# Kernel tuning notes

Hardware: AMD Instinct MI355X
Metric: run time of the kernel (lower is better)

The kernel has to match this reference:

```python
import math
import jax, jax.numpy as jnp
import numpy as np

B, S, E, H = 4, 2048, 1024, 16
HD = E // H  # 64


def setup_inputs() -> dict:
    key = jax.random.key(0)
    ks = jax.random.split(key, 7)
    scale = 1.0 / math.sqrt(E)
    return {
        "x": jax.random.normal(ks[0], (B, S, E), dtype=jnp.float32),
        "Wq": jax.random.normal(ks[1], (H, HD, E), dtype=jnp.float32) * scale,
        "bq": jax.random.normal(ks[2], (H, HD), dtype=jnp.float32) * 0.01,
        "Wk": jax.random.normal(ks[3], (H, HD, E), dtype=jnp.float32) * scale,
        "bk": jax.random.normal(ks[4], (H, HD), dtype=jnp.float32) * 0.01,
        "Wv": jax.random.normal(ks[5], (H, HD, E), dtype=jnp.float32) * scale,
        "bv": jax.random.normal(ks[6], (H, HD), dtype=jnp.float32) * 0.01,
    }


def reference(x, Wq, bq, Wk, bk, Wv, bv):
    b, s, e = x.shape
    h, hd, _ = Wq.shape
    inv_scale = 1.0 / math.sqrt(hd)
    # per-head linear projections (torch Linear: x @ W^T + b), batched over heads
    q = jnp.einsum("bse,hde->bshd", x, Wq) + bq  # [B,S,H,HD]
    k = jnp.einsum("bse,hde->bshd", x, Wk) + bk
    v = jnp.einsum("bse,hde->bshd", x, Wv) + bv
    # causal mask: -inf above diagonal (added before scaling, as in source;
    # -inf * inv_scale is still -inf so math is identical)
    mask = jnp.triu(jnp.full((s, s), -jnp.inf, dtype=x.dtype), k=1)
    scores = (jnp.einsum("bqhd,bkhd->bhqk", q, k) + mask) * inv_scale  # [B,H,S,S]
    attn = jax.nn.softmax(scores, axis=-1)
    out = jnp.einsum("bhqk,bkhd->bqhd", attn, v)  # [B,S,H,HD]
    # concat over heads in head order == reshape with head-major last dims
    return out.reshape(b, s, h * hd)
```

## Files before the change

### kernel.cpp

```cpp
#include <hip/hip_runtime.h>


typedef __bf16 bf16x8 __attribute__((ext_vector_type(8)));
typedef __bf16 bf16x4 __attribute__((ext_vector_type(4)));
typedef float f32x4 __attribute__((ext_vector_type(4)));
typedef unsigned short us8 __attribute__((ext_vector_type(8)));
typedef unsigned short us4 __attribute__((ext_vector_type(4)));

#define Bb 4
#define Ss 2048
#define Ee 1024
#define Hh 16
#define HD 64

#if __has_builtin(__builtin_amdgcn_exp2f)
#define EXP2(x) __builtin_amdgcn_exp2f(x)
#else
#define EXP2(x) exp2f(x)
#endif

__device__ __forceinline__ unsigned short f2bf(float f) {
  union { float f; unsigned u; } v; v.f = f;
  unsigned u = v.u;
  u += 0x7fffu + ((u >> 16) & 1u);
  return (unsigned short)(u >> 16);
}

__device__ __forceinline__ void gl_lds16(const void* g, void* l) {
  __builtin_amdgcn_global_load_lds((const __attribute__((address_space(1))) void*)g,
                                   (__attribute__((address_space(3))) void*)l, 16, 0, 0);
}

#define DSR(d, a, o) asm volatile("ds_read_b128 %0, %1 offset:" #o : "=v"(d) : "v"(a))
#define DSW(a, d, o) asm volatile("ds_write_b64 %0, %1 offset:" #o :: "v"(a), "v"(d) : "memory")
#define LGKM0 asm volatile("s_waitcnt lgkmcnt(0)" ::: "memory"); __builtin_amdgcn_sched_barrier(0)
#define LGKM8 asm volatile("s_waitcnt lgkmcnt(8)" ::: "memory"); __builtin_amdgcn_sched_barrier(0)

__global__ __launch_bounds__(256) void cvt_all(const float* __restrict__ x,
                                               const float* __restrict__ wq,
                                               const float* __restrict__ wk,
                                               const float* __restrict__ wv,
                                               unsigned short* __restrict__ xb,
                                               unsigned short* __restrict__ wb) {
  int i = blockIdx.x * 256 + threadIdx.x;
  const float* src; unsigned short* dst; int idx;
  if (i < 2097152)      { src = x;  dst = xb;                idx = i; }
  else if (i < 2359296) { src = wq; dst = wb;                idx = i - 2097152; }
  else if (i < 2621440) { src = wk; dst = wb + 1048576;      idx = i - 2359296; }
  else                  { src = wv; dst = wb + 2 * 1048576;  idx = i - 2621440; }
  float4 f = ((const float4*)src)[idx];
  us4 o = { f2bf(f.x), f2bf(f.y), f2bf(f.z), f2bf(f.w) };
  ((us4*)dst)[idx] = o;
}

__global__ __launch_bounds__(256, 2) void qkv_gemm(const unsigned short* __restrict__ xb,
                                                   const unsigned short* __restrict__ wb_all,
                                                   const float* __restrict__ bq,
                                                   const float* __restrict__ bk,
                                                   const float* __restrict__ bv,
                                                   unsigned short* __restrict__ qkv) {
  const int z = blockIdx.z;
  const unsigned short* wb = wb_all + (size_t)z * (Ee * Ee);
  const float* bias = (z == 0) ? bq : (z == 1) ? bk : bv;
  unsigned short* outb = qkv + (size_t)z * (Bb * Ss * Ee);
  const float osc = (z == 0) ? 0.180336880f : 1.0f;

  __shared__ unsigned short SMEM[32768];

  const int t = threadIdx.x;
  const int wave = t >> 6, lane = t & 63, quad = lane >> 4, ln = lane & 15;
  const int wr = wave >> 1, wc = wave & 1;
  const int m0 = blockIdx.x * 128, n0 = blockIdx.y * 128;

  const int r32 = t >> 3;
  const int cs = ((t & 7) ^ (r32 & 7)) * 8;
  const int t8 = t * 8;
  const unsigned short* gA0 = xb + (size_t)(m0 + r32) * Ee + cs;
  const unsigned short* gA1 = gA0 + 64 * Ee;
  const unsigned short* gB0 = wb + (size_t)(n0 + r32) * Ee + cs;
  const unsigned short* gB1 = gB0 + 64 * Ee;

  const int swz0 = ((0 * 4 + quad) ^ (ln & 7)) * 16;
  const int swz1 = ((1 * 4 + quad) ^ (ln & 7)) * 16;
  int aA0 = (wr * 32 + ln) * 128 + swz0;
  int aA1 = (wr * 32 + ln) * 128 + swz1;
  int bA0 = 16384 + (wc * 32 + ln) * 128 + swz0;
  int bA1 = 16384 + (wc * 32 + ln) * 128 + swz1;

  f32x4 acc[2][2][2][2] = {};
  bf16x8 af0[2][2], af1[2][2], bf0[2][2], bf1[2][2];

  gl_lds16(gA0,           &SMEM[t8]);
  gl_lds16(gA0 + 32 * Ee, &SMEM[t8 + 2048]);
  gl_lds16(gB0,           &SMEM[8192 + t8]);
  gl_lds16(gB0 + 32 * Ee, &SMEM[8192 + t8 + 2048]);
  gl_lds16(gB1,           &SMEM[12288 + t8]);
  gl_lds16(gB1 + 32 * Ee, &SMEM[12288 + t8 + 2048]);
  gl_lds16(gA1,           &SMEM[4096 + t8]);
  gl_lds16(gA1 + 32 * Ee, &SMEM[4096 + t8 + 2048]);

#pragma unroll 1
  for (int kt = 0; kt < 15; ++kt) {
    const int sbuf = ((kt & 1) << 14) ^ 16384;
    const int co = (kt + 1) * 64;

    gl_lds16(gA0 + co,           &SMEM[sbuf + t8]);
    gl_lds16(gA0 + co + 32 * Ee, &SMEM[sbuf + t8 + 2048]);
    gl_lds16(gB0 + co,           &SMEM[sbuf + 8192 + t8]);
    gl_lds16(gB0 + co + 32 * Ee, &SMEM[sbuf + 8192 + t8 + 2048]);
    gl_lds16(gB1 + co,           &SMEM[sbuf + 12288 + t8]);
    gl_lds16(gB1 + co + 32 * Ee, &SMEM[sbuf + 12288 + t8 + 2048]);
    gl_lds16(gA1 + co,           &SMEM[sbuf + 4096 + t8]);
    gl_lds16(gA1 + co + 32 * Ee, &SMEM[sbuf + 4096 + t8 + 2048]);

    asm volatile("s_waitcnt vmcnt(8)" ::: "memory");
    asm volatile("s_barrier" ::: "memory");

    DSR(af0[0][0], aA0, 0);    DSR(af0[1][0], aA0, 2048);
    DSR(af0[0][1], aA1, 0);    DSR(af0[1][1], aA1, 2048);
    DSR(bf0[0][0], bA0, 0);    DSR(bf0[1][0], bA0, 2048);
    DSR(bf0[0][1], bA1, 0);    DSR(bf0[1][1], bA1, 2048);
    DSR(af1[0][0], aA0, 8192); DSR(af1[1][0], aA0, 10240);
    DSR(af1[0][1], aA1, 8192); DSR(af1[1][1], aA1, 10240);
    DSR(bf1[0][0], bA0, 8192); DSR(bf1[1][0], bA0, 10240);
    DSR(bf1[0][1], bA1, 8192); DSR(bf1[1][1], bA1, 10240);
    LGKM8;
    __builtin_amdgcn_s_setprio(1);
#pragma unroll
    for (int kk = 0; kk < 2; ++kk)
#pragma unroll
      for (int i = 0; i < 2; ++i)
#pragma unroll
        for (int j = 0; j < 2; ++j)
          acc[0][0][i][j] = __builtin_amdgcn_mfma_f32_16x16x32_bf16(af0[i][kk], bf0[j][kk], acc[0][0][i][j], 0, 0, 0);
    LGKM0;
#pragma unroll
    for (int kk = 0; kk < 2; ++kk)
#pragma unroll
      for (int i = 0; i < 2; ++i)
#pragma unroll
        for (int j = 0; j < 2; ++j)
          acc[0][1][i][j] = __builtin_amdgcn_mfma_f32_16x16x32_bf16(af0[i][kk], bf1[j][kk], acc[0][1][i][j], 0, 0, 0);
#pragma unroll
    for (int kk = 0; kk < 2; ++kk)
#pragma unroll
      for (int i = 0; i < 2; ++i)
#pragma unroll
        for (int j = 0; j < 2; ++j)
          acc[1][0][i][j] = __builtin_amdgcn_mfma_f32_16x16x32_bf16(af1[i][kk], bf0[j][kk], acc[1][0][i][j], 0, 0, 0);
#pragma unroll
    for (int kk = 0; kk < 2; ++kk)
#pragma unroll
      for (int i = 0; i < 2; ++i)
#pragma unroll
        for (int j = 0; j < 2; ++j)
          acc[1][1][i][j] = __builtin_amdgcn_mfma_f32_16x16x32_bf16(af1[i][kk], bf1[j][kk], acc[1][1][i][j], 0, 0, 0);
    __builtin_amdgcn_s_setprio(0);
    __builtin_amdgcn_sched_barrier(0);
    asm volatile("s_barrier" ::: "memory");

    aA0 ^= 32768; aA1 ^= 32768; bA0 ^= 32768; bA1 ^= 32768;
  }

  {
    asm volatile("s_waitcnt vmcnt(0)" ::: "memory");
    asm volatile("s_barrier" ::: "memory");
    DSR(af0[0][0], aA0, 0);    DSR(af0[1][0], aA0, 2048);
    DSR(af0[0][1], aA1, 0);    DSR(af0[1][1], aA1, 2048);
    DSR(bf0[0][0], bA0, 0);    DSR(bf0[1][0], bA0, 2048);
    DSR(bf0[0][1], bA1, 0);    DSR(bf0[1][1], bA1, 2048);
    DSR(af1[0][0], aA0, 8192); DSR(af1[1][0], aA0, 10240);
    DSR(af1[0][1], aA1, 8192); DSR(af1[1][1], aA1, 10240);
    DSR(bf1[0][0], bA0, 8192); DSR(bf1[1][0], bA0, 10240);
    DSR(bf1[0][1], bA1, 8192); DSR(bf1[1][1], bA1, 10240);
    LGKM8;
#pragma unroll
    for (int kk = 0; kk < 2; ++kk)
#pragma unroll
      for (int i = 0; i < 2; ++i)
#pragma unroll
        for (int j = 0; j < 2; ++j)
          acc[0][0][i][j] = __builtin_amdgcn_mfma_f32_16x16x32_bf16(af0[i][kk], bf0[j][kk], acc[0][0][i][j], 0, 0, 0);
    LGKM0;
#pragma unroll
    for (int kk = 0; kk < 2; ++kk)
#pragma unroll
      for (int i = 0; i < 2; ++i)
#pragma unroll
        for (int j = 0; j < 2; ++j)
          acc[0][1][i][j] = __builtin_amdgcn_mfma_f32_16x16x32_bf16(af0[i][kk], bf1[j][kk], acc[0][1][i][j], 0, 0, 0);
#pragma unroll
    for (int kk = 0; kk < 2; ++kk)
#pragma unroll
      for (int i = 0; i < 2; ++i)
#pragma unroll
        for (int j = 0; j < 2; ++j)
          acc[1][0][i][j] = __builtin_amdgcn_mfma_f32_16x16x32_bf16(af1[i][kk], bf0[j][kk], acc[1][0][i][j], 0, 0, 0);
#pragma unroll
    for (int kk = 0; kk < 2; ++kk)
#pragma unroll
      for (int i = 0; i < 2; ++i)
#pragma unroll
        for (int j = 0; j < 2; ++j)
          acc[1][1][i][j] = __builtin_amdgcn_mfma_f32_16x16x32_bf16(af1[i][kk], bf1[j][kk], acc[1][1][i][j], 0, 0, 0);
    __builtin_amdgcn_sched_barrier(0);
  }

  float biasj[2][2];
#pragma unroll
  for (int qb = 0; qb < 2; ++qb)
#pragma unroll
    for (int j = 0; j < 2; ++j)
      biasj[qb][j] = bias[n0 + qb * 64 + wc * 32 + j * 16 + ln];

  if (z != 2) {
#pragma unroll
    for (int qa = 0; qa < 2; ++qa)
#pragma unroll
      for (int qb = 0; qb < 2; ++qb)
#pragma unroll
        for (int i = 0; i < 2; ++i)
#pragma unroll
          for (int j = 0; j < 2; ++j)
#pragma unroll
            for (int r = 0; r < 4; ++r) {
              int m = m0 + qa * 64 + wr * 32 + i * 16 + quad * 4 + r;
              int n = n0 + qb * 64 + wc * 32 + j * 16 + ln;
              int b_ = m >> 11, s = m & 2047;
              int h = n >> 6, d = n & 63;
              outb[(((size_t)b_ * Hh + h) * Ss + s) * HD + d] =
                  f2bf((acc[qa][qb][i][j][r] + biasj[qb][j]) * osc);
            }
  } else {
    __syncthreads();
#pragma unroll
    for (int qa = 0; qa < 2; ++qa)
#pragma unroll
      for (int qb = 0; qb < 2; ++qb)
#pragma unroll
        for (int i = 0; i < 2; ++i)
#pragma unroll
          for (int j = 0; j < 2; ++j)
#pragma unroll
            for (int r = 0; r < 4; ++r) {
              int nc = qb * 64 + wc * 32 + j * 16 + ln;
              int mr = qa * 64 + wr * 32 + i * 16 + quad * 4 + r;
              SMEM[nc * 136 + mr] = f2bf(acc[qa][qb][i][j][r] + biasj[qb][j]);
            }
    __syncthreads();
    int nr = t >> 1, mh = t & 1;
    int n = n0 + nr, h = n >> 6, d = n & 63;
    int b_ = m0 >> 11;
    int s0 = (m0 & 2047) + mh * 64;
#pragma unroll
    for (int q = 0; q < 8; ++q) {
      us8 vdat = *(const us8*)&SMEM[nr * 136 + mh * 64 + q * 8];
      *(us8*)&outb[(((size_t)b_ * Hh + h) * HD + d) * Ss + s0 + q * 8] = vdat;
    }
  }
}

__global__ __launch_bounds__(512, 2) void flash_attn(const unsigned short* __restrict__ qkv,
                                                     float* __restrict__ out) {
  const int id = blockIdx.x;
  const int bh = id & 63;
  const int p = id >> 6;
  const int b_ = bh >> 4, h = bh & 15;

  const unsigned short* qb  = qkv + (size_t)bh * (Ss * HD);
  const unsigned short* kb  = qkv + (size_t)(64 + bh) * (Ss * HD);
  const unsigned short* vtb = qkv + (size_t)(128 + bh) * (Ss * HD);

  __shared__ __bf16 LDS[25600];

  const int t = threadIdx.x;
  const int wave = t >> 6, lane = t & 63, quad = lane >> 4, ln = lane & 15;
  const int uw = wave >> 2;

  const int r6 = t >> 3;
  const int cstage = ((t & 7) ^ (r6 & 7)) * 8;
  const int t8 = t * 8;

  const int qts[2] = { 15 - p, p };
  const int KTB = 2 * qts[0] + 2;
  const int su0 = 2 * qts[0] + uw;
  const int su1 = 2 * qts[1] + uw;
  const int qrow0 = qts[0] * 128 + wave * 16 + ln;
  const int qrow1 = qts[1] * 128 + wave * 16 + ln;

  int ka0 = ln * 128 + ((quad ^ (ln & 7)) * 16);
  int ka1 = ln * 128 + (((4 + quad) ^ (ln & 7)) * 16);
  const int pw = (16384 + (wave * 16 + ln) * 72 + quad * 4) * 2;
  const int pr = (16384 + (wave * 16 + ln) * 72 + quad * 8) * 2;

  bf16x8 qf[2][2];
#pragma unroll
  for (int qt = 0; qt < 2; ++qt)
#pragma unroll
    for (int ks = 0; ks < 2; ++ks)
      qf[qt][ks] = *(const bf16x8*)(qb + (size_t)(qts[qt] * 128 + wave * 16 + ln) * HD +
                                    ks * 32 + quad * 8);

  bf16x8 onef;
#pragma unroll
  for (int j = 0; j < 8; ++j) onef[j] = (__bf16)1.0f;

  f32x4 o[2][4] = {};
  f32x4 l4[2] = {};

  auto body = [&](int kt) {
    if (kt > su0) return;
    const bool a1 = (kt <= su1);
    const int k0 = kt * 64;
    f32x4 s0[4] = {}, s1[4] = {};
    bf16x8 kf[2][2];

    DSR(kf[0][0], ka0, 0);    DSR(kf[1][0], ka0, 2048);
    DSR(kf[0][1], ka1, 0);    DSR(kf[1][1], ka1, 2048);
    LGKM0;
#pragma unroll
    for (int ks = 0; ks < 2; ++ks) {
      s0[0] = __builtin_amdgcn_mfma_f32_16x16x32_bf16(kf[0][ks], qf[0][ks], s0[0], 0, 0, 0);
      s0[1] = __builtin_amdgcn_mfma_f32_16x16x32_bf16(kf[1][ks], qf[0][ks], s0[1], 0, 0, 0);
    }
    if (a1)
#pragma unroll
      for (int ks = 0; ks < 2; ++ks) {
        s1[0] = __builtin_amdgcn_mfma_f32_16x16x32_bf16(kf[0][ks], qf[1][ks], s1[0], 0, 0, 0);
        s1[1] = __builtin_amdgcn_mfma_f32_16x16x32_bf16(kf[1][ks], qf[1][ks], s1[1], 0, 0, 0);
      }
    DSR(kf[0][0], ka0, 4096); DSR(kf[1][0], ka0, 6144);
    DSR(kf[0][1], ka1, 4096); DSR(kf[1][1], ka1, 6144);
    LGKM0;
#pragma unroll
    for (int ks = 0; ks < 2; ++ks) {
      s0[2] = __builtin_amdgcn_mfma_f32_16x16x32_bf16(kf[0][ks], qf[0][ks], s0[2], 0, 0, 0);
      s0[3] = __builtin_amdgcn_mfma_f32_16x16x32_bf16(kf[1][ks], qf[0][ks], s0[3], 0, 0, 0);
    }
    if (a1)
#pragma unroll
      for (int ks = 0; ks < 2; ++ks) {
        s1[2] = __builtin_amdgcn_mfma_f32_16x16x32_bf16(kf[0][ks], qf[1][ks], s1[2], 0, 0, 0);
        s1[3] = __builtin_amdgcn_mfma_f32_16x16x32_bf16(kf[1][ks], qf[1][ks], s1[3], 0, 0, 0);
      }

    if (kt == su0) {
#pragma unroll
      for (int g = 0; g < 4; ++g)
#pragma unroll
        for (int r = 0; r < 4; ++r) {
          int kcol = k0 + g * 16 + quad * 4 + r;
          if (kcol > qrow0) s0[g][r] = -__builtin_inff();
        }
    }
    {
      bf16x4 pk;
      pk = bf16x4{ (__bf16)EXP2(s0[0][0]), (__bf16)EXP2(s0[0][1]), (__bf16)EXP2(s0[0][2]), (__bf16)EXP2(s0[0][3]) };
      DSW(pw, pk, 0);
      pk = bf16x4{ (__bf16)EXP2(s0[1][0]), (__bf16)EXP2(s0[1][1]), (__bf16)EXP2(s0[1][2]), (__bf16)EXP2(s0[1][3]) };
      DSW(pw, pk, 32);
      pk = bf16x4{ (__bf16)EXP2(s0[2][0]), (__bf16)EXP2(s0[2][1]), (__bf16)EXP2(s0[2][2]), (__bf16)EXP2(s0[2][3]) };
      DSW(pw, pk, 64);
      pk = bf16x4{ (__bf16)EXP2(s0[3][0]), (__bf16)EXP2(s0[3][1]), (__bf16)EXP2(s0[3][2]), (__bf16)EXP2(s0[3][3]) };
      DSW(pw, pk, 96);
    }
    bf16x8 pf0[2], pf1[2];
    DSR(pf0[0], pr, 0); DSR(pf0[1], pr, 64);
    LGKM0;

    if (a1) {
      if (kt == su1) {
#pragma unroll
        for (int g = 0; g < 4; ++g)
#pragma unroll
          for (int r = 0; r < 4; ++r) {
            int kcol = k0 + g * 16 + quad * 4 + r;
            if (kcol > qrow1) s1[g][r] = -__builtin_inff();
          }
      }
      bf16x4 pk;
      pk = bf16x4{ (__bf16)EXP2(s1[0][0]), (__bf16)EXP2(s1[0][1]), (__bf16)EXP2(s1[0][2]), (__bf16)EXP2(s1[0][3]) };
      DSW(pw, pk, 0);
      pk = bf16x4{ (__bf16)EXP2(s1[1][0]), (__bf16)EXP2(s1[1][1]), (__bf16)EXP2(s1[1][2]), (__bf16)EXP2(s1[1][3]) };
      DSW(pw, pk, 32);
      pk = bf16x4{ (__bf16)EXP2(s1[2][0]), (__bf16)EXP2(s1[2][1]), (__bf16)EXP2(s1[2][2]), (__bf16)EXP2(s1[2][3]) };
      DSW(pw, pk, 64);
      pk = bf16x4{ (__bf16)EXP2(s1[3][0]), (__bf16)EXP2(s1[3][1]), (__bf16)EXP2(s1[3][2]), (__bf16)EXP2(s1[3][3]) };
      DSW(pw, pk, 96);
      DSR(pf1[0], pr, 0); DSR(pf1[1], pr, 64);
      LGKM0;
    }

    l4[0] = __builtin_amdgcn_mfma_f32_16x16x32_bf16(pf0[0], onef, l4[0], 0, 0, 0);
    l4[0] = __builtin_amdgcn_mfma_f32_16x16x32_bf16(pf0[1], onef, l4[0], 0, 0, 0);
    if (a1) {
      l4[1] = __builtin_amdgcn_mfma_f32_16x16x32_bf16(pf1[0], onef, l4[1], 0, 0, 0);
      l4[1] = __builtin_amdgcn_mfma_f32_16x16x32_bf16(pf1[1], onef, l4[1], 0, 0, 0);
    }

    DSR(kf[0][0], ka0, 16384); DSR(kf[1][0], ka0, 18432);
    DSR(kf[0][1], ka1, 16384); DSR(kf[1][1], ka1, 18432);
    LGKM0;
#pragma unroll
    for (int ks = 0; ks < 2; ++ks) {
      o[0][0] = __builtin_amdgcn_mfma_f32_16x16x32_bf16(pf0[ks], kf[0][ks], o[0][0], 0, 0, 0);
      o[0][1] = __builtin_amdgcn_mfma_f32_16x16x32_bf16(pf0[ks], kf[1][ks], o[0][1], 0, 0, 0);
    }
    if (a1)
#pragma unroll
      for (int ks = 0; ks < 2; ++ks) {
        o[1][0] = __builtin_amdgcn_mfma_f32_16x16x32_bf16(pf1[ks], kf[0][ks], o[1][0], 0, 0, 0);
        o[1][1] = __builtin_amdgcn_mfma_f32_16x16x32_bf16(pf1[ks], kf[1][ks], o[1][1], 0, 0, 0);
      }
    DSR(kf[0][0], ka0, 20480); DSR(kf[1][0], ka0, 22528);
    DSR(kf[0][1], ka1, 20480); DSR(kf[1][1], ka1, 22528);
    LGKM0;
#pragma unroll
    for (int ks = 0; ks < 2; ++ks) {
      o[0][2] = __builtin_amdgcn_mfma_f32_16x16x32_bf16(pf0[ks], kf[0][ks], o[0][2], 0, 0, 0);
      o[0][3] = __builtin_amdgcn_mfma_f32_16x16x32_bf16(pf0[ks], kf[1][ks], o[0][3], 0, 0, 0);
    }
    if (a1)
#pragma unroll
      for (int ks = 0; ks < 2; ++ks) {
        o[1][2] = __builtin_amdgcn_mfma_f32_16x16x32_bf16(pf1[ks], kf[0][ks], o[1][2], 0, 0, 0);
        o[1][3] = __builtin_amdgcn_mfma_f32_16x16x32_bf16(pf1[ks], kf[1][ks], o[1][3], 0, 0, 0);
      }
  };

  gl_lds16(kb + r6 * HD + cstage,  &LDS[t8]);
  gl_lds16(vtb + r6 * Ss + cstage, &LDS[8192 + t8]);

#pragma unroll 1
  for (int kt = 0; kt < KTB - 1; ++kt) {
    const int sb = (kt & 1) ^ 1;
    gl_lds16(kb + (size_t)(kt + 1) * (64 * HD) + r6 * HD + cstage, &LDS[sb * 4096 + t8]);
    gl_lds16(vtb + (kt + 1) * 64 + r6 * Ss + cstage,               &LDS[8192 + sb * 4096 + t8]);
    asm volatile("s_waitcnt vmcnt(2)" ::: "memory");
    asm volatile("s_barrier" ::: "memory");
    body(kt);
    asm volatile("s_barrier" ::: "memory");
    ka0 ^= 8192; ka1 ^= 8192;
  }
  asm volatile("s_waitcnt vmcnt(0)" ::: "memory");
  asm volatile("s_barrier" ::: "memory");
  body(KTB - 1);

#pragma unroll
  for (int qt = 0; qt < 2; ++qt) {
    float linv[4];
#pragma unroll
    for (int r = 0; r < 4; ++r) linv[r] = 1.0f / l4[qt][r];
#pragma unroll
    for (int g = 0; g < 4; ++g)
#pragma unroll
      for (int r = 0; r < 4; ++r) {
        int orow = qts[qt] * 128 + wave * 16 + quad * 4 + r;
        out[((size_t)b_ * Ss + orow) * Ee + h * HD + g * 16 + ln] = o[qt][g][r] * linv[r];
      }
  }
}

extern "C" void kernel_launch(void* const* d_in, const int* in_sizes, int n_in,
                              void* d_out, int out_size, void* d_ws, size_t ws_size,
                              hipStream_t stream) {
  const float* x  = (const float*)d_in[0];
  const float* Wq = (const float*)d_in[1];
  const float* bq = (const float*)d_in[2];
  const float* Wk = (const float*)d_in[3];
  const float* bk = (const float*)d_in[4];
  const float* Wv = (const float*)d_in[5];
  const float* bv = (const float*)d_in[6];
  float* out = (float*)d_out;

  unsigned short* ws  = (unsigned short*)d_ws;
  unsigned short* xb  = ws;
  unsigned short* wb  = ws + 8388608;
  unsigned short* qkv = ws + 8388608 + 3 * 1048576;

  cvt_all<<<11264, 256, 0, stream>>>(x, Wq, Wk, Wv, xb, wb);
  qkv_gemm<<<dim3(64, 8, 3), 256, 0, stream>>>(xb, wb, bq, bk, bv, qkv);
  flash_attn<<<512, 512, 0, stream>>>(qkv, out);
}
```

Measured before the change: 195.3 us.

## Triple-buffer K/V tiles in LDS to prefetch two tiles ahead

Moves the flash-attention K and V^T staging from double to triple buffering in shared memory. Global-to-LDS loads are now issued two iterations ahead with a rotating buffer offset, and the wait count is relaxed so more load latency is hidden behind MFMA work. The cost is more LDS per block (about 66KB instead of 50KB), which may limit occupancy at two blocks per CU. The P scratch region and the V read offsets are shifted to fit the new layout.

```diff
diff --git a/kernel.cpp b/kernel.cpp
--- a/kernel.cpp
+++ b/kernel.cpp
@@ -271,7 +271,7 @@
   const unsigned short* kb  = qkv + (size_t)(64 + bh) * (Ss * HD);
   const unsigned short* vtb = qkv + (size_t)(128 + bh) * (Ss * HD);
 
-  __shared__ __bf16 LDS[25600];
+  __shared__ __bf16 LDS[33792];
 
   const int t = threadIdx.x;
   const int wave = t >> 6, lane = t & 63, quad = lane >> 4, ln = lane & 15;
@@ -288,10 +288,10 @@
   const int qrow0 = qts[0] * 128 + wave * 16 + ln;
   const int qrow1 = qts[1] * 128 + wave * 16 + ln;
 
-  int ka0 = ln * 128 + ((quad ^ (ln & 7)) * 16);
-  int ka1 = ln * 128 + (((4 + quad) ^ (ln & 7)) * 16);
-  const int pw = (16384 + (wave * 16 + ln) * 72 + quad * 4) * 2;
-  const int pr = (16384 + (wave * 16 + ln) * 72 + quad * 8) * 2;
+  const int ka0l = ln * 128 + ((quad ^ (ln & 7)) * 16);
+  const int ka1l = ln * 128 + (((4 + quad) ^ (ln & 7)) * 16);
+  const int pw = 49152 + (wave * 16 + ln) * 144 + quad * 8;
+  const int pr = 49152 + (wave * 16 + ln) * 144 + quad * 16;
 
   bf16x8 qf[2][2];
 #pragma unroll
@@ -308,15 +308,15 @@
   f32x4 o[2][4] = {};
   f32x4 l4[2] = {};
 
-  auto body = [&](int kt) {
+  auto body = [&](int kt, int kaA, int kaB) {
     if (kt > su0) return;
     const bool a1 = (kt <= su1);
     const int k0 = kt * 64;
     f32x4 s0[4] = {}, s1[4] = {};
     bf16x8 kf[2][2];
 
-    DSR(kf[0][0], ka0, 0);    DSR(kf[1][0], ka0, 2048);
-    DSR(kf[0][1], ka1, 0);    DSR(kf[1][1], ka1, 2048);
+    DSR(kf[0][0], kaA, 0);    DSR(kf[1][0], kaA, 2048);
+    DSR(kf[0][1], kaB, 0);    DSR(kf[1][1], kaB, 2048);
     LGKM0;
 #pragma unroll
     for (int ks = 0; ks < 2; ++ks) {
@@ -329,8 +329,8 @@
         s1[0] = __builtin_amdgcn_mfma_f32_16x16x32_bf16(kf[0][ks], qf[1][ks], s1[0], 0, 0, 0);
         s1[1] = __builtin_amdgcn_mfma_f32_16x16x32_bf16(kf[1][ks], qf[1][ks], s1[1], 0, 0, 0);
       }
-    DSR(kf[0][0], ka0, 4096); DSR(kf[1][0], ka0, 6144);
-    DSR(kf[0][1], ka1, 4096); DSR(kf[1][1], ka1, 6144);
+    DSR(kf[0][0], kaA, 4096); DSR(kf[1][0], kaA, 6144);
+    DSR(kf[0][1], kaB, 4096); DSR(kf[1][1], kaB, 6144);
     LGKM0;
 #pragma unroll
     for (int ks = 0; ks < 2; ++ks) {
@@ -398,8 +398,8 @@
       l4[1] = __builtin_amdgcn_mfma_f32_16x16x32_bf16(pf1[1], onef, l4[1], 0, 0, 0);
     }
 
-    DSR(kf[0][0], ka0, 16384); DSR(kf[1][0], ka0, 18432);
-    DSR(kf[0][1], ka1, 16384); DSR(kf[1][1], ka1, 18432);
+    DSR(kf[0][0], kaA, 24576); DSR(kf[1][0], kaA, 26624);
+    DSR(kf[0][1], kaB, 24576); DSR(kf[1][1], kaB, 26624);
     LGKM0;
 #pragma unroll
     for (int ks = 0; ks < 2; ++ks) {
@@ -412,8 +412,8 @@
         o[1][0] = __builtin_amdgcn_mfma_f32_16x16x32_bf16(pf1[ks], kf[0][ks], o[1][0], 0, 0, 0);
         o[1][1] = __builtin_amdgcn_mfma_f32_16x16x32_bf16(pf1[ks], kf[1][ks], o[1][1], 0, 0, 0);
       }
-    DSR(kf[0][0], ka0, 20480); DSR(kf[1][0], ka0, 22528);
-    DSR(kf[0][1], ka1, 20480); DSR(kf[1][1], ka1, 22528);
+    DSR(kf[0][0], kaA, 28672); DSR(kf[1][0], kaA, 30720);
+    DSR(kf[0][1], kaB, 28672); DSR(kf[1][1], kaB, 30720);
     LGKM0;
 #pragma unroll
     for (int ks = 0; ks < 2; ++ks) {
@@ -428,23 +428,33 @@
       }
   };
 
-  gl_lds16(kb + r6 * HD + cstage,  &LDS[t8]);
-  gl_lds16(vtb + r6 * Ss + cstage, &LDS[8192 + t8]);
-
+  gl_lds16(kb + r6 * HD + cstage,             &LDS[t8]);
+  gl_lds16(vtb + r6 * Ss + cstage,            &LDS[12288 + t8]);
+  gl_lds16(kb + 64 * HD + r6 * HD + cstage,   &LDS[4096 + t8]);
+  gl_lds16(vtb + 64 + r6 * Ss + cstage,       &LDS[12288 + 4096 + t8]);
+
+  int cOff = 0;
+  int sOff = 16384;
 #pragma unroll 1
-  for (int kt = 0; kt < KTB - 1; ++kt) {
-    const int sb = (kt & 1) ^ 1;
-    gl_lds16(kb + (size_t)(kt + 1) * (64 * HD) + r6 * HD + cstage, &LDS[sb * 4096 + t8]);
-    gl_lds16(vtb + (kt + 1) * 64 + r6 * Ss + cstage,               &LDS[8192 + sb * 4096 + t8]);
-    asm volatile("s_waitcnt vmcnt(2)" ::: "memory");
+  for (int kt = 0; kt < KTB - 2; ++kt) {
+    const int sE = sOff >> 1;
+    gl_lds16(kb + (size_t)(kt + 2) * (64 * HD) + r6 * HD + cstage, &LDS[sE + t8]);
+    gl_lds16(vtb + (kt + 2) * 64 + r6 * Ss + cstage,               &LDS[12288 + sE + t8]);
+    asm volatile("s_waitcnt vmcnt(4)" ::: "memory");
     asm volatile("s_barrier" ::: "memory");
-    body(kt);
+    body(kt, ka0l + cOff, ka1l + cOff);
     asm volatile("s_barrier" ::: "memory");
-    ka0 ^= 8192; ka1 ^= 8192;
+    cOff = (cOff == 16384) ? 0 : cOff + 8192;
+    sOff = (sOff == 16384) ? 0 : sOff + 8192;
   }
+  asm volatile("s_waitcnt vmcnt(2)" ::: "memory");
+  asm volatile("s_barrier" ::: "memory");
+  body(KTB - 2, ka0l + cOff, ka1l + cOff);
+  asm volatile("s_barrier" ::: "memory");
+  cOff = (cOff == 16384) ? 0 : cOff + 8192;
   asm volatile("s_waitcnt vmcnt(0)" ::: "memory");
   asm volatile("s_barrier" ::: "memory");
-  body(KTB - 1);
+  body(KTB - 1, ka0l + cOff, ka1l + cOff);
 
 #pragma unroll
   for (int qt = 0; qt < 2; ++qt) {
```

Measured after the change: 204.9 us. +4.9%, slower.
